# Performance work log

Hardware: AMD Instinct MI355X
Metric: run time of the kernel (lower is better)

Reference implementation:

```python
import jax, jax.numpy as jnp
import numpy as np

BLOCK_SIZE = 256


def setup_inputs() -> dict:
    key = jax.random.key(0)
    k1, k2, k3, k4 = jax.random.split(key, 4)
    B, T, C, H = 512, 256, 384, 64
    x = jax.random.normal(k1, (B, T, C), dtype=jnp.float32)
    Wk = jax.random.normal(k2, (H, C), dtype=jnp.float32) * (1.0 / np.sqrt(C))
    Wq = jax.random.normal(k3, (H, C), dtype=jnp.float32) * (1.0 / np.sqrt(C))
    Wv = jax.random.normal(k4, (H, C), dtype=jnp.float32) * (1.0 / np.sqrt(C))
    return {"x": x, "Wk": Wk, "Wq": Wq, "Wv": Wv}


def reference(x, Wk, Wq, Wv):
    # x: [B, T, C]; Wk/Wq/Wv: [H, C] (torch nn.Linear weight layout, bias=False)
    B, T, C = x.shape
    H = Wk.shape[0]
    k = jnp.einsum('btc,hc->bth', x, Wk)
    q = jnp.einsum('btc,hc->bth', x, Wq)
    v = jnp.einsum('btc,hc->bth', x, Wv)
    scale = 1.0 / jnp.sqrt(jnp.float32(H))
    scores = jnp.einsum('bqh,bkh->bqk', q, k) * scale  # [B, T, T]
    causal = jnp.tril(jnp.ones((T, T), dtype=bool))
    scores = jnp.where(causal, scores, -jnp.inf)
    weights = jax.nn.softmax(scores, axis=-1)
    # dropout is identity in eval mode
    out = jnp.einsum('bqk,bkh->bqh', weights, v)  # [B, T, H]
    return out
```

## Files before the change

### kernel.cpp

```cpp
#include <hip/hip_runtime.h>
#include <hip/hip_bf16.h>
#include <math.h>

#define TT 256
#define CC 384
#define HH 64

typedef float v4f  __attribute__((ext_vector_type(4)));
typedef short short8 __attribute__((ext_vector_type(8)));

#define MFMA(a, b, c) __builtin_amdgcn_mfma_f32_16x16x32_bf16((a), (b), (c), 0, 0, 0)

__device__ __forceinline__ unsigned short f2bf(float f) {
    unsigned int u = __float_as_uint(f);
    u += 0x7FFFu + ((u >> 16) & 1u);
    return (unsigned short)(u >> 16);
}

#define OFF_Q  0
#define OFF_K  18432
#define OFF_VT 36864
#define OFF_X  53760
#define OFF_W  64000
#define SMEM_BYTES (71680 * 2)

__global__ __launch_bounds__(512, 2)
void head_fused(const float* __restrict__ x, const float* __restrict__ Wkp,
                const float* __restrict__ Wqp, const float* __restrict__ Wvp,
                float* __restrict__ out)
{
    extern __shared__ unsigned short sm[];
    unsigned short* q_s  = sm + OFF_Q;
    unsigned short* k_s  = sm + OFF_K;
    unsigned short* vt_s = sm + OFF_VT;
    unsigned short* x_s  = sm + OFF_X;
    unsigned short* w_s  = sm + OFF_W;

    const int b    = blockIdx.x;
    const int tid  = threadIdx.x;
    const int wave = tid >> 6;
    const int lane = tid & 63;
    const int col  = lane & 15;
    const int quad = lane >> 4;

    const float* xb = x + (size_t)b * TT * CC;

    const int lrow = tid >> 3;
    const int lc4  = (tid & 7) * 4;

    const float* xp0 = xb  + lrow * CC + lc4;
    const float* wq0 = Wqp + lrow * CC + lc4;
    const float* wk0 = Wkp + lrow * CC + lc4;
    const float* wv0 = Wvp + lrow * CC + lc4;

    v4f acc[2][12];
    #pragma unroll
    for (int i = 0; i < 2; ++i)
        #pragma unroll
        for (int j = 0; j < 12; ++j)
            acc[i][j] = (v4f){0.f, 0.f, 0.f, 0.f};

    float4 xA[4]; float4 wA[3];
    #pragma unroll
    for (int i = 0; i < 4; ++i) xA[i] = *(const float4*)(xp0 + i * 64 * CC);
    wA[0] = *(const float4*)(wq0);
    wA[1] = *(const float4*)(wk0);
    wA[2] = *(const float4*)(wv0);

    const int mrow0 = ((wave * 2 + 0) * 16 + col) * 40 + quad * 8;
    const int mrow1 = ((wave * 2 + 1) * 16 + col) * 40 + quad * 8;

    #pragma unroll
    for (int s = 0; s < 12; ++s) {
        float4 xB[4]; float4 wB[3];
        if (s + 1 < 12) {
            const int k0 = (s + 1) * 32;
            #pragma unroll
            for (int i = 0; i < 4; ++i) xB[i] = *(const float4*)(xp0 + i * 64 * CC + k0);
            wB[0] = *(const float4*)(wq0 + k0);
            wB[1] = *(const float4*)(wk0 + k0);
            wB[2] = *(const float4*)(wv0 + k0);
        }
        __syncthreads();
        #pragma unroll
        for (int i = 0; i < 4; ++i) {
            ushort4 u;
            u.x = f2bf(xA[i].x); u.y = f2bf(xA[i].y);
            u.z = f2bf(xA[i].z); u.w = f2bf(xA[i].w);
            *(ushort4*)&x_s[(i * 64 + lrow) * 40 + lc4] = u;
        }
        #pragma unroll
        for (int i = 0; i < 3; ++i) {
            ushort4 u;
            u.x = f2bf(wA[i].x); u.y = f2bf(wA[i].y);
            u.z = f2bf(wA[i].z); u.w = f2bf(wA[i].w);
            *(ushort4*)&w_s[(i * 64 + lrow) * 40 + lc4] = u;
        }
        __syncthreads();
        short8 a0 = *(const short8*)&x_s[mrow0];
        short8 a1 = *(const short8*)&x_s[mrow1];
        #pragma unroll
        for (int nt = 0; nt < 12; ++nt) {
            short8 bf = *(const short8*)&w_s[(nt * 16 + col) * 40 + quad * 8];
            acc[0][nt] = MFMA(a0, bf, acc[0][nt]);
            acc[1][nt] = MFMA(a1, bf, acc[1][nt]);
        }
        if (s + 1 < 12) {
            #pragma unroll
            for (int i = 0; i < 4; ++i) xA[i] = xB[i];
            #pragma unroll
            for (int i = 0; i < 3; ++i) wA[i] = wB[i];
        }
    }

    #pragma unroll
    for (int mi = 0; mi < 2; ++mi) {
        const int mt = wave * 2 + mi;
        #pragma unroll
        for (int nt = 0; nt < 12; ++nt) {
            #pragma unroll
            for (int r = 0; r < 4; ++r) {
                const int t = mt * 16 + quad * 4 + r;
                const int n = nt * 16 + col;
                const unsigned short hv = f2bf(acc[mi][nt][r]);
                if (n < 64)       q_s[t * 72 + n] = hv;
                else if (n < 128) k_s[t * 72 + (n - 64)] = hv;
                else              vt_s[(n - 128) * 264 + t] = hv;
            }
        }
    }
    __syncthreads();

    const float scale = 0.125f;

    #pragma unroll
    for (int mi = 0; mi < 2; ++mi) {
        const int mt = mi ? (15 - wave) : wave;
        const int qoff = (mt * 16 + col) * 72 + quad * 8;
        const short8 aq0 = *(const short8*)&q_s[qoff];
        const short8 aq1 = *(const short8*)&q_s[qoff + 32];

        float m_i[4], l_i[4];
        v4f oacc[4];
        #pragma unroll
        for (int r = 0; r < 4; ++r) { m_i[r] = -INFINITY; l_i[r] = 0.f; }
        #pragma unroll
        for (int hn = 0; hn < 4; ++hn) oacc[hn] = (v4f){0.f, 0.f, 0.f, 0.f};

        unsigned short* Pb = x_s + wave * 16 * 40;
        const int nch = mt / 2 + 1;

        for (int kc = 0; kc < nch; ++kc) {
            const int kb = kc * 32;
            v4f s0 = (v4f){0.f, 0.f, 0.f, 0.f};
            v4f s1 = (v4f){0.f, 0.f, 0.f, 0.f};
            {
                const int ko0 = (kb + col) * 72 + quad * 8;
                const int ko1 = (kb + 16 + col) * 72 + quad * 8;
                short8 b00 = *(const short8*)&k_s[ko0];
                short8 b01 = *(const short8*)&k_s[ko0 + 32];
                short8 b10 = *(const short8*)&k_s[ko1];
                short8 b11 = *(const short8*)&k_s[ko1 + 32];
                s0 = MFMA(aq0, b00, s0);
                s0 = MFMA(aq1, b01, s0);
                s1 = MFMA(aq0, b10, s1);
                s1 = MFMA(aq1, b11, s1);
            }
            const bool diag = (kc == mt / 2);
            #pragma unroll
            for (int r = 0; r < 4; ++r) {
                const int t = mt * 16 + quad * 4 + r;
                float v0 = s0[r] * scale;
                float v1 = s1[r] * scale;
                if (diag) {
                    if (kb + col > t)      v0 = -1e30f;
                    if (kb + 16 + col > t) v1 = -1e30f;
                }
                float cm = fmaxf(v0, v1);
                cm = fmaxf(cm, __shfl_xor(cm, 1));
                cm = fmaxf(cm, __shfl_xor(cm, 2));
                cm = fmaxf(cm, __shfl_xor(cm, 4));
                cm = fmaxf(cm, __shfl_xor(cm, 8));
                const float mo = m_i[r];
                const float mn = fmaxf(mo, cm);
                const float al = __expf(mo - mn);
                m_i[r] = mn;
                const float p0 = __expf(v0 - mn);
                const float p1 = __expf(v1 - mn);
                float rs = p0 + p1;
                rs += __shfl_xor(rs, 1);
                rs += __shfl_xor(rs, 2);
                rs += __shfl_xor(rs, 4);
                rs += __shfl_xor(rs, 8);
                l_i[r] = l_i[r] * al + rs;
                #pragma unroll
                for (int hn = 0; hn < 4; ++hn) oacc[hn][r] *= al;
                Pb[(quad * 4 + r) * 40 + col]      = f2bf(p0);
                Pb[(quad * 4 + r) * 40 + 16 + col] = f2bf(p1);
            }
            __threadfence_block();
            const short8 ap = *(const short8*)&Pb[col * 40 + quad * 8];
            #pragma unroll
            for (int hn = 0; hn < 4; ++hn) {
                short8 bv = *(const short8*)&vt_s[(hn * 16 + col) * 264 + kb + quad * 8];
                oacc[hn] = MFMA(ap, bv, oacc[hn]);
            }
        }

        #pragma unroll
        for (int r = 0; r < 4; ++r) {
            const int t = mt * 16 + quad * 4 + r;
            const float inv = 1.0f / l_i[r];
            float* op = out + ((size_t)b * TT + t) * HH;
            #pragma unroll
            for (int hn = 0; hn < 4; ++hn)
                op[hn * 16 + col] = oacc[hn][r] * inv;
        }
    }
}

extern "C" void kernel_launch(void* const* d_in, const int* in_sizes, int n_in,
                              void* d_out, int out_size, void* d_ws, size_t ws_size,
                              hipStream_t stream) {
    const float* x  = (const float*)d_in[0];
    const float* Wk = (const float*)d_in[1];
    const float* Wq = (const float*)d_in[2];
    const float* Wv = (const float*)d_in[3];
    float* out = (float*)d_out;

    (void)hipFuncSetAttribute((const void*)head_fused,
                              hipFuncAttributeMaxDynamicSharedMemorySize, SMEM_BYTES);

    head_fused<<<dim3(512), dim3(512), SMEM_BYTES, stream>>>(x, Wk, Wq, Wv, out);
}
```

Baseline: 354.1 us.

## Split fused head kernel into QKV projection and attention kernels via workspace

Replaces the single fused per-batch kernel with two kernels. The first projects 128-row tiles of x into bf16 Q, K and transposed V in global workspace, using small static LDS so more blocks can be resident. The second runs causal attention with 1024 blocks of 256 threads, each covering half the query tiles of one batch, and reads K and V fragments directly from global memory. This aims to raise occupancy and parallelism, at the cost of a global round trip for Q/K/V and a second launch.

Measured after the change: 348.1 us. Within noise of the previous version (-1.7%).

```diff
diff --git a/kernel.cpp b/kernel.cpp
--- a/kernel.cpp
+++ b/kernel.cpp
@@ -6,7 +6,7 @@
 #define CC 384
 #define HH 64
 
-typedef float v4f  __attribute__((ext_vector_type(4)));
+typedef float v4f   __attribute__((ext_vector_type(4)));
 typedef short short8 __attribute__((ext_vector_type(8)));
 
 #define MFMA(a, b, c) __builtin_amdgcn_mfma_f32_16x16x32_bf16((a), (b), (c), 0, 0, 0)
@@ -17,128 +17,139 @@
     return (unsigned short)(u >> 16);
 }
 
-#define OFF_Q  0
-#define OFF_K  18432
-#define OFF_VT 36864
-#define OFF_X  53760
-#define OFF_W  64000
-#define SMEM_BYTES (71680 * 2)
-
-__global__ __launch_bounds__(512, 2)
-void head_fused(const float* __restrict__ x, const float* __restrict__ Wkp,
-                const float* __restrict__ Wqp, const float* __restrict__ Wvp,
-                float* __restrict__ out)
+__global__ __launch_bounds__(512, 4)
+void qkv_proj(const float* __restrict__ x, const float* __restrict__ Wkp,
+              const float* __restrict__ Wqp, const float* __restrict__ Wvp,
+              unsigned short* __restrict__ qg, unsigned short* __restrict__ kg,
+              unsigned short* __restrict__ vtg)
 {
-    extern __shared__ unsigned short sm[];
-    unsigned short* q_s  = sm + OFF_Q;
-    unsigned short* k_s  = sm + OFF_K;
-    unsigned short* vt_s = sm + OFF_VT;
-    unsigned short* x_s  = sm + OFF_X;
-    unsigned short* w_s  = sm + OFF_W;
-
-    const int b    = blockIdx.x;
+    __shared__ unsigned short sm[26112];
+    unsigned short* x_s    = sm;
+    unsigned short* w_s    = sm + 5120;
+    unsigned short* epi_qk = sm;
+    unsigned short* epi_vt = sm + 17408;
+
     const int tid  = threadIdx.x;
     const int wave = tid >> 6;
     const int lane = tid & 63;
     const int col  = lane & 15;
     const int quad = lane >> 4;
-
-    const float* xb = x + (size_t)b * TT * CC;
-
-    const int lrow = tid >> 3;
-    const int lc4  = (tid & 7) * 4;
-
-    const float* xp0 = xb  + lrow * CC + lc4;
-    const float* wq0 = Wqp + lrow * CC + lc4;
-    const float* wk0 = Wkp + lrow * CC + lc4;
-    const float* wv0 = Wvp + lrow * CC + lc4;
-
-    v4f acc[2][12];
-    #pragma unroll
-    for (int i = 0; i < 2; ++i)
-        #pragma unroll
-        for (int j = 0; j < 12; ++j)
-            acc[i][j] = (v4f){0.f, 0.f, 0.f, 0.f};
-
-    float4 xA[4]; float4 wA[3];
-    #pragma unroll
-    for (int i = 0; i < 4; ++i) xA[i] = *(const float4*)(xp0 + i * 64 * CC);
-    wA[0] = *(const float4*)(wq0);
-    wA[1] = *(const float4*)(wk0);
-    wA[2] = *(const float4*)(wv0);
-
-    const int mrow0 = ((wave * 2 + 0) * 16 + col) * 40 + quad * 8;
-    const int mrow1 = ((wave * 2 + 1) * 16 + col) * 40 + quad * 8;
+    const int row0 = blockIdx.x * 128;
+
+    const int lr  = tid >> 3;
+    const int lc4 = (tid & 7) * 4;
+
+    const float* xp  = x   + (size_t)(row0 + lr) * CC + lc4;
+    const float* wqp = Wqp + (size_t)lr * CC + lc4;
+    const float* wkp = Wkp + (size_t)lr * CC + lc4;
+    const float* wvp = Wvp + (size_t)lr * CC + lc4;
+
+    v4f acc[12];
+    #pragma unroll
+    for (int j = 0; j < 12; ++j) acc[j] = (v4f){0.f, 0.f, 0.f, 0.f};
+
+    float4 xA0 = *(const float4*)(xp);
+    float4 xA1 = *(const float4*)(xp + 64 * CC);
+    float4 wqA = *(const float4*)(wqp);
+    float4 wkA = *(const float4*)(wkp);
+    float4 wvA = *(const float4*)(wvp);
+
+    const int afrag_off = (wave * 16 + col) * 40 + quad * 8;
 
     #pragma unroll
     for (int s = 0; s < 12; ++s) {
-        float4 xB[4]; float4 wB[3];
-        if (s + 1 < 12) {
+        float4 xB0, xB1, wqB, wkB, wvB;
+        if (s < 11) {
             const int k0 = (s + 1) * 32;
-            #pragma unroll
-            for (int i = 0; i < 4; ++i) xB[i] = *(const float4*)(xp0 + i * 64 * CC + k0);
-            wB[0] = *(const float4*)(wq0 + k0);
-            wB[1] = *(const float4*)(wk0 + k0);
-            wB[2] = *(const float4*)(wv0 + k0);
+            xB0 = *(const float4*)(xp + k0);
+            xB1 = *(const float4*)(xp + 64 * CC + k0);
+            wqB = *(const float4*)(wqp + k0);
+            wkB = *(const float4*)(wkp + k0);
+            wvB = *(const float4*)(wvp + k0);
         }
         __syncthreads();
-        #pragma unroll
-        for (int i = 0; i < 4; ++i) {
+        {
             ushort4 u;
-            u.x = f2bf(xA[i].x); u.y = f2bf(xA[i].y);
-            u.z = f2bf(xA[i].z); u.w = f2bf(xA[i].w);
-            *(ushort4*)&x_s[(i * 64 + lrow) * 40 + lc4] = u;
-        }
-        #pragma unroll
-        for (int i = 0; i < 3; ++i) {
-            ushort4 u;
-            u.x = f2bf(wA[i].x); u.y = f2bf(wA[i].y);
-            u.z = f2bf(wA[i].z); u.w = f2bf(wA[i].w);
-            *(ushort4*)&w_s[(i * 64 + lrow) * 40 + lc4] = u;
+            u.x = f2bf(xA0.x); u.y = f2bf(xA0.y); u.z = f2bf(xA0.z); u.w = f2bf(xA0.w);
+            *(ushort4*)&x_s[lr * 40 + lc4] = u;
+            u.x = f2bf(xA1.x); u.y = f2bf(xA1.y); u.z = f2bf(xA1.z); u.w = f2bf(xA1.w);
+            *(ushort4*)&x_s[(lr + 64) * 40 + lc4] = u;
+            u.x = f2bf(wqA.x); u.y = f2bf(wqA.y); u.z = f2bf(wqA.z); u.w = f2bf(wqA.w);
+            *(ushort4*)&w_s[lr * 40 + lc4] = u;
+            u.x = f2bf(wkA.x); u.y = f2bf(wkA.y); u.z = f2bf(wkA.z); u.w = f2bf(wkA.w);
+            *(ushort4*)&w_s[(64 + lr) * 40 + lc4] = u;
+            u.x = f2bf(wvA.x); u.y = f2bf(wvA.y); u.z = f2bf(wvA.z); u.w = f2bf(wvA.w);
+            *(ushort4*)&w_s[(128 + lr) * 40 + lc4] = u;
         }
         __syncthreads();
-        short8 a0 = *(const short8*)&x_s[mrow0];
-        short8 a1 = *(const short8*)&x_s[mrow1];
+        const short8 a = *(const short8*)&x_s[afrag_off];
         #pragma unroll
         for (int nt = 0; nt < 12; ++nt) {
-            short8 bf = *(const short8*)&w_s[(nt * 16 + col) * 40 + quad * 8];
-            acc[0][nt] = MFMA(a0, bf, acc[0][nt]);
-            acc[1][nt] = MFMA(a1, bf, acc[1][nt]);
-        }
-        if (s + 1 < 12) {
-            #pragma unroll
-            for (int i = 0; i < 4; ++i) xA[i] = xB[i];
-            #pragma unroll
-            for (int i = 0; i < 3; ++i) wA[i] = wB[i];
-        }
-    }
+            const short8 bf = *(const short8*)&w_s[(nt * 16 + col) * 40 + quad * 8];
+            acc[nt] = MFMA(a, bf, acc[nt]);
+        }
+        if (s < 11) { xA0 = xB0; xA1 = xB1; wqA = wqB; wkA = wkB; wvA = wvB; }
+    }
+
+    __syncthreads();
+    #pragma unroll
+    for (int nt = 0; nt < 12; ++nt) {
+        #pragma unroll
+        for (int r = 0; r < 4; ++r) {
+            const int rl = wave * 16 + quad * 4 + r;
+            const int n  = nt * 16 + col;
+            const unsigned short hv = f2bf(acc[nt][r]);
+            if (nt < 8) epi_qk[rl * 136 + n] = hv;
+            else        epi_vt[(n - 128) * 136 + rl] = hv;
+        }
+    }
+    __syncthreads();
+
+    const int b    = row0 >> 8;
+    const int half = (row0 >> 7) & 1;
+
+    #pragma unroll
+    for (int p = 0; p < 4; ++p) {
+        const int idx = tid + p * 512;
+        const int r = idx >> 4, ch = idx & 15;
+        const short8 v = *(const short8*)&epi_qk[r * 136 + ch * 8];
+        const size_t base = (size_t)(row0 + r) * 64 + (ch & 7) * 8;
+        if (ch < 8) *(short8*)&qg[base] = v;
+        else        *(short8*)&kg[base] = v;
+    }
+    #pragma unroll
+    for (int p = 0; p < 2; ++p) {
+        const int idx = tid + p * 512;
+        const int h = idx >> 4, ch = idx & 15;
+        const short8 v = *(const short8*)&epi_vt[h * 136 + ch * 8];
+        *(short8*)&vtg[((size_t)b * 64 + h) * 256 + half * 128 + ch * 8] = v;
+    }
+}
+
+__global__ __launch_bounds__(256)
+void attn(const unsigned short* __restrict__ qg, const unsigned short* __restrict__ kg,
+          const unsigned short* __restrict__ vtg, float* __restrict__ out)
+{
+    __shared__ unsigned short Pb_all[4 * 16 * 40];
+    const int tid  = threadIdx.x;
+    const int wave = tid >> 6;
+    const int lane = tid & 63;
+    const int col  = lane & 15;
+    const int quad = lane >> 4;
+    const int b    = blockIdx.x >> 1;
+    const int qh   = blockIdx.x & 1;
+
+    unsigned short* Pb = Pb_all + wave * 640;
+    const unsigned short* kb_base = kg  + (size_t)b * 256 * 64;
+    const unsigned short* vt_base = vtg + (size_t)b * 64 * 256;
+    const float scale = 0.125f;
 
     #pragma unroll
     for (int mi = 0; mi < 2; ++mi) {
-        const int mt = wave * 2 + mi;
-        #pragma unroll
-        for (int nt = 0; nt < 12; ++nt) {
-            #pragma unroll
-            for (int r = 0; r < 4; ++r) {
-                const int t = mt * 16 + quad * 4 + r;
-                const int n = nt * 16 + col;
-                const unsigned short hv = f2bf(acc[mi][nt][r]);
-                if (n < 64)       q_s[t * 72 + n] = hv;
-                else if (n < 128) k_s[t * 72 + (n - 64)] = hv;
-                else              vt_s[(n - 128) * 264 + t] = hv;
-            }
-        }
-    }
-    __syncthreads();
-
-    const float scale = 0.125f;
-
-    #pragma unroll
-    for (int mi = 0; mi < 2; ++mi) {
-        const int mt = mi ? (15 - wave) : wave;
-        const int qoff = (mt * 16 + col) * 72 + quad * 8;
-        const short8 aq0 = *(const short8*)&q_s[qoff];
-        const short8 aq1 = *(const short8*)&q_s[qoff + 32];
+        const int qt = qh * 8 + (mi ? (7 - wave) : wave);
+        const size_t qoff = ((size_t)b * 256 + qt * 16 + col) * 64 + quad * 8;
+        const short8 aq0 = *(const short8*)(qg + qoff);
+        const short8 aq1 = *(const short8*)(qg + qoff + 32);
 
         float m_i[4], l_i[4];
         v4f oacc[4];
@@ -147,29 +158,27 @@
         #pragma unroll
         for (int hn = 0; hn < 4; ++hn) oacc[hn] = (v4f){0.f, 0.f, 0.f, 0.f};
 
-        unsigned short* Pb = x_s + wave * 16 * 40;
-        const int nch = mt / 2 + 1;
-
+        const int nch = qt / 2 + 1;
         for (int kc = 0; kc < nch; ++kc) {
             const int kb = kc * 32;
             v4f s0 = (v4f){0.f, 0.f, 0.f, 0.f};
             v4f s1 = (v4f){0.f, 0.f, 0.f, 0.f};
             {
-                const int ko0 = (kb + col) * 72 + quad * 8;
-                const int ko1 = (kb + 16 + col) * 72 + quad * 8;
-                short8 b00 = *(const short8*)&k_s[ko0];
-                short8 b01 = *(const short8*)&k_s[ko0 + 32];
-                short8 b10 = *(const short8*)&k_s[ko1];
-                short8 b11 = *(const short8*)&k_s[ko1 + 32];
+                const int ko0 = (kb + col) * 64 + quad * 8;
+                const int ko1 = (kb + 16 + col) * 64 + quad * 8;
+                const short8 b00 = *(const short8*)(kb_base + ko0);
+                const short8 b01 = *(const short8*)(kb_base + ko0 + 32);
+                const short8 b10 = *(const short8*)(kb_base + ko1);
+                const short8 b11 = *(const short8*)(kb_base + ko1 + 32);
                 s0 = MFMA(aq0, b00, s0);
                 s0 = MFMA(aq1, b01, s0);
                 s1 = MFMA(aq0, b10, s1);
                 s1 = MFMA(aq1, b11, s1);
             }
-            const bool diag = (kc == mt / 2);
+            const bool diag = (kc == qt / 2);
             #pragma unroll
             for (int r = 0; r < 4; ++r) {
-                const int t = mt * 16 + quad * 4 + r;
+                const int t = qt * 16 + quad * 4 + r;
                 float v0 = s0[r] * scale;
                 float v1 = s1[r] * scale;
                 if (diag) {
@@ -202,14 +211,14 @@
             const short8 ap = *(const short8*)&Pb[col * 40 + quad * 8];
             #pragma unroll
             for (int hn = 0; hn < 4; ++hn) {
-                short8 bv = *(const short8*)&vt_s[(hn * 16 + col) * 264 + kb + quad * 8];
+                const short8 bv = *(const short8*)(vt_base + (hn * 16 + col) * 256 + kb + quad * 8);
                 oacc[hn] = MFMA(ap, bv, oacc[hn]);
             }
         }
 
         #pragma unroll
         for (int r = 0; r < 4; ++r) {
-            const int t = mt * 16 + quad * 4 + r;
+            const int t = qt * 16 + quad * 4 + r;
             const float inv = 1.0f / l_i[r];
             float* op = out + ((size_t)b * TT + t) * HH;
             #pragma unroll
@@ -228,8 +237,10 @@
     const float* Wv = (const float*)d_in[3];
     float* out = (float*)d_out;
 
-    (void)hipFuncSetAttribute((const void*)head_fused,
-                              hipFuncAttributeMaxDynamicSharedMemorySize, SMEM_BYTES);
-
-    head_fused<<<dim3(512), dim3(512), SMEM_BYTES, stream>>>(x, Wk, Wq, Wv, out);
-}
+    unsigned short* qg  = (unsigned short*)d_ws;
+    unsigned short* kg  = qg + (size_t)512 * 256 * 64;
+    unsigned short* vtg = kg + (size_t)512 * 256 * 64;
+
+    qkv_proj<<<dim3(1024), dim3(512), 0, stream>>>(x, Wk, Wq, Wv, qg, kg, vtg);
+    attn<<<dim3(1024), dim3(256), 0, stream>>>(qg, kg, vtg, out);
+}
```
